# Kernel tuning notes

Measured on AMD Instinct MI355X. Metric: run time of the kernel, lower is better.

## Reference

```python
import jax, jax.numpy as jnp
import numpy as np
from jax import lax

NPOINT = 1024
NSAMPLE = 64
RADIUS = 0.2
EPS = 1e-5  # BatchNorm eps


def farthest_point_sample(xyz, npoint):
    # xyz: [B, N, 3] -> idx [B, npoint]; deterministic init at point 0
    B, N, _ = xyz.shape

    def step(carry, _):
        dist, farthest = carry
        centroid = jnp.take_along_axis(xyz, farthest[:, None, None], axis=1)  # [B,1,3]
        d = jnp.sum((xyz - centroid) ** 2, axis=-1)  # [B,N]
        dist = jnp.minimum(dist, d)
        new_far = jnp.argmax(dist, axis=-1).astype(jnp.int32)
        return (dist, new_far), farthest

    init = (jnp.full((B, N), 1e10, xyz.dtype), jnp.zeros((B,), jnp.int32))
    _, idxs = lax.scan(step, init, None, length=npoint)
    return jnp.transpose(idxs)  # [B, npoint]


def square_distance(src, dst):
    # src [B,S,3], dst [B,N,3] -> [B,S,N]
    d = -2.0 * jnp.einsum('bsc,bnc->bsn', src, dst)
    d += jnp.sum(src ** 2, -1)[:, :, None]
    d += jnp.sum(dst ** 2, -1)[:, None, :]
    return d


def query_ball_point(radius, nsample, xyz, new_xyz):
    B, N, _ = xyz.shape
    sqr = square_distance(new_xyz, xyz)  # [B,S,N]
    gi = jnp.where(sqr > radius ** 2, N, jnp.arange(N, dtype=jnp.int32))
    gi = jnp.sort(gi, axis=-1)[:, :, :nsample]  # [B,S,K]
    first = gi[:, :, :1]
    gi = jnp.where(gi == N, first, gi)
    return gi


def mlp_bn_relu(x, W, g, b):
    # x [B,S,K,Cin], W [Cin,Cout]; 1x1 conv + training-mode BN + ReLU
    y = jnp.einsum('bskc,co->bsko', x, W)
    m = jnp.mean(y, axis=(0, 1, 2))
    v = jnp.var(y, axis=(0, 1, 2))
    y = (y - m) * lax.rsqrt(v + EPS) * g + b
    return jax.nn.relu(y)


def setup_inputs() -> dict:
    key = jax.random.key(0)
    ks = jax.random.split(key, 8)
    B, N, C = 8, 4096, 128
    xyz = jax.random.uniform(ks[0], (B, N, 3), dtype=jnp.float32)
    features = jax.random.normal(ks[1], (B, C, N), dtype=jnp.float32)
    c_in = C + 3  # use_xyz
    W1 = jax.random.normal(ks[2], (c_in, 128), dtype=jnp.float32) * 0.05
    W2 = jax.random.normal(ks[3], (128, 128), dtype=jnp.float32) * 0.05
    W3 = jax.random.normal(ks[4], (128, 256), dtype=jnp.float32) * 0.05
    return {
        'xyz': xyz, 'features': features,
        'W1': W1, 'g1': jnp.ones((128,)), 'b1': jnp.zeros((128,)),
        'W2': W2, 'g2': jnp.ones((128,)), 'b2': jnp.zeros((128,)),
        'W3': W3, 'g3': jnp.ones((256,)), 'b3': jnp.zeros((256,)),
    }


def reference(xyz, features, W1, g1, b1, W2, g2, b2, W3, g3, b3):
    fps_idx = farthest_point_sample(xyz, NPOINT)              # [B,S]
    new_xyz = jnp.take_along_axis(xyz, fps_idx[:, :, None], axis=1)  # [B,S,3]
    gi = query_ball_point(RADIUS, NSAMPLE, xyz, new_xyz)      # [B,S,K]
    gather = jax.vmap(lambda p, i: p[i])                      # per-batch gather
    grouped_xyz = gather(xyz, gi) - new_xyz[:, :, None, :]    # [B,S,K,3]
    grouped_feat = gather(jnp.transpose(features, (0, 2, 1)), gi)  # [B,S,K,C]
    x = jnp.concatenate([grouped_xyz, grouped_feat], axis=-1)  # [B,S,K,3+C]
    x = mlp_bn_relu(x, W1, g1, b1)
    x = mlp_bn_relu(x, W2, g2, b2)
    x = mlp_bn_relu(x, W3, g3, b3)
    new_features = jnp.transpose(jnp.max(x, axis=2), (0, 2, 1))  # [B,256,S]
    return new_xyz, new_features
```

## Files before the change

### kernel.cpp

```cpp
#include <hip/hip_runtime.h>

#define B_  8
#define N_  4096
#define S_  1024
#define K_  64
#define CF_ 128
#define M_  (B_*S_*K_)

typedef __attribute__((ext_vector_type(8))) short bshort8;
typedef __attribute__((ext_vector_type(4))) float f32x4;
typedef __attribute__((ext_vector_type(4))) int   i32x4;
typedef __attribute__((ext_vector_type(2))) float f32x2;
typedef __attribute__((ext_vector_type(4))) unsigned short us4;

__device__ __forceinline__ unsigned short f2bf(float f){
  unsigned int u = __float_as_uint(f);
  u = u + 0x7FFFu + ((u >> 16) & 1u);
  return (unsigned short)(u >> 16);
}
__device__ __forceinline__ float bf2f(unsigned short h){
  return __uint_as_float(((unsigned int)h) << 16);
}

__global__ __launch_bounds__(256) void prep_kernel(const float* __restrict__ f,
                                                   const float* __restrict__ W1,
                                                   const float* __restrict__ W2,
                                                   const float* __restrict__ W3,
                                                   unsigned short* __restrict__ ft,
                                                   unsigned short* __restrict__ Wt1,
                                                   unsigned short* __restrict__ Wt2,
                                                   unsigned short* __restrict__ Wt3){
  __shared__ float tile[32][33];
  const int blk = blockIdx.x;
  if (blk < 4096){
    int nt = blk & 127, ct = (blk>>7)&3, b = blk>>9;
    int tx = threadIdx.x & 31, ty = threadIdx.x >> 5;
#pragma unroll
    for (int r=0; r<32; r+=8)
      tile[ty+r][tx] = f[((size_t)(b*128 + ct*32 + ty + r))*4096 + nt*32 + tx];
    __syncthreads();
#pragma unroll
    for (int r=0; r<32; r+=8){
      int n = nt*32 + ty + r, cc = ct*32 + tx;
      ft[((size_t)b*4096 + n)*128 + cc] = f2bf(tile[tx][ty+r]);
    }
  } else {
    int t = (blk-4096)*256 + threadIdx.x;
    int stride = 64*256;
    for (int idx=t; idx<128*160; idx+=stride){
      int n = idx/160, k = idx-(idx/160)*160;
      float v = 0.f;
      if (k < 128) v = W1[(k+3)*128 + n];
      else if (k < 131) v = W1[(k-128)*128 + n];
      Wt1[idx] = f2bf(v);
    }
    for (int idx=t; idx<128*128; idx+=stride){
      int n = idx>>7, k = idx&127;
      Wt2[idx] = f2bf(W2[k*128+n]);
    }
    for (int idx=t; idx<256*128; idx+=stride){
      int n = idx>>7, k = idx&127;
      Wt3[idx] = f2bf(W3[k*256+n]);
    }
  }
}

__global__ __launch_bounds__(256,2) void pgemm_kernel(const unsigned short* __restrict__ featT,
                                                      const unsigned short* __restrict__ Wt1,
                                                      float* __restrict__ P){
  __shared__ alignas(16) unsigned short At[128*40];
  __shared__ alignas(16) unsigned short Bt[128*40];
  const int t = threadIdx.x, blk = blockIdx.x;
  const size_t rowBase = (size_t)blk*128;
  const int lane = t&63, wave = t>>6;
  const int wm = wave>>1, wn = wave&1;
  const int lrow = lane&15, quad = lane>>4;
  f32x4 acc[4][4];
  const f32x4 z4 = {0.f,0.f,0.f,0.f};
#pragma unroll
  for (int i=0;i<4;++i)
#pragma unroll
    for (int j=0;j<4;++j) acc[i][j]=z4;
  for (int ch=0; ch<4; ++ch){
    __syncthreads();
#pragma unroll
    for (int half=0; half<2; ++half){
      int sl = t + half*256; int r = sl>>2, p = sl&3;
      *(bshort8*)&At[r*40+p*8] = *(const bshort8*)(featT + (rowBase + r)*CF_ + ch*32 + p*8);
      *(bshort8*)&Bt[r*40+p*8] = *(const bshort8*)(Wt1 + r*160 + ch*32 + p*8);
    }
    __syncthreads();
    bshort8 af[4], bfr[4];
#pragma unroll
    for (int mt=0; mt<4; ++mt) af[mt]  = *(const bshort8*)&At[(wm*64+mt*16+lrow)*40 + quad*8];
#pragma unroll
    for (int nt=0; nt<4; ++nt) bfr[nt] = *(const bshort8*)&Bt[(wn*64+nt*16+lrow)*40 + quad*8];
#pragma unroll
    for (int mt=0; mt<4; ++mt)
#pragma unroll
      for (int nt=0; nt<4; ++nt)
        acc[mt][nt] = __builtin_amdgcn_mfma_f32_16x16x32_bf16(af[mt], bfr[nt], acc[mt][nt], 0,0,0);
  }
#pragma unroll
  for (int mt=0; mt<4; ++mt)
#pragma unroll
    for (int nt=0; nt<4; ++nt)
#pragma unroll
      for (int r=0; r<4; ++r){
        int row = wm*64 + mt*16 + quad*4 + r;
        int col = wn*64 + nt*16 + lrow;
        P[(rowBase + row)*128 + col] = acc[mt][nt][r];
      }
}

#define DPP_PAIR_STEP(CTRL)                                                     \
  {                                                                             \
    int _vi = __builtin_amdgcn_update_dpp(__float_as_int(best), __float_as_int(best), (CTRL), 0xF, 0xF, false); \
    int _ii = __builtin_amdgcn_update_dpp(bidx, bidx, (CTRL), 0xF, 0xF, false); \
    float _ov = __int_as_float(_vi);                                            \
    bool _tk = (_ov > best) || (_ov == best && _ii < bidx);                     \
    best = _tk ? _ov : best;                                                    \
    bidx = _tk ? _ii : bidx;                                                    \
  }

__global__ __launch_bounds__(256) void fps_kernel(const float* __restrict__ xyz,
                                                  float* __restrict__ nx_out,
                                                  float* __restrict__ nx_ws){
#pragma clang fp contract(off)
  __shared__ float sx[N_], sy[N_], sz[N_];
  __shared__ int   sidx[S_];
  __shared__ alignas(16) float redv[2][4];
  __shared__ alignas(16) int   redi[2][4];
  const int b = blockIdx.x, t = threadIdx.x;
  const int lane = t & 63, w = t >> 6;
  const float* xb = xyz + (size_t)b*N_*3;
  f32x2 px[8], py[8], pz[8], dist[8];
#pragma unroll
  for (int j=0;j<8;++j){
    int i0 = (2*j)*256 + t, i1 = (2*j+1)*256 + t;
    float x0=xb[i0*3+0], y0=xb[i0*3+1], z0=xb[i0*3+2];
    float x1=xb[i1*3+0], y1=xb[i1*3+1], z1=xb[i1*3+2];
    px[j] = (f32x2){x0,x1}; py[j] = (f32x2){y0,y1}; pz[j] = (f32x2){z0,z1};
    dist[j] = (f32x2){1e10f,1e10f};
    sx[i0]=x0; sy[i0]=y0; sz[i0]=z0;
    sx[i1]=x1; sy[i1]=y1; sz[i1]=z1;
  }
  __syncthreads();
  int farthest = 0;
  float cx = xb[0], cy = xb[1], cz = xb[2];
  for (int it=0; it<S_; ++it){
    if (t==0) sidx[it] = farthest;
    f32x2 cx2 = (f32x2){cx,cx}, cy2 = (f32x2){cy,cy}, cz2 = (f32x2){cz,cz};
    float best = -1.0f; int bidx = 0;
#pragma unroll
    for (int j=0;j<8;++j){
      f32x2 dx = px[j] - cx2;
      f32x2 dy = py[j] - cy2;
      f32x2 dz = pz[j] - cz2;
      f32x2 d  = (dx*dx + dy*dy) + dz*dz;
      f32x2 nd;
      nd.x = fminf(dist[j].x, d.x);
      nd.y = fminf(dist[j].y, d.y);
      dist[j] = nd;
      bool tk0 = nd.x > best;
      best = tk0 ? nd.x : best;
      bidx = tk0 ? ((2*j)*256 + t) : bidx;
      bool tk1 = nd.y > best;
      best = tk1 ? nd.y : best;
      bidx = tk1 ? ((2*j+1)*256 + t) : bidx;
    }
    DPP_PAIR_STEP(0xB1);
    DPP_PAIR_STEP(0x4E);
    DPP_PAIR_STEP(0x124);
    DPP_PAIR_STEP(0x128);
    DPP_PAIR_STEP(0x142);
    DPP_PAIR_STEP(0x143);
    const int buf = it & 1;
    if (lane == 63){ redv[buf][w] = best; redi[buf][w] = bidx; }
    __syncthreads();
    f32x4 vv = *(const f32x4*)&redv[buf][0];
    i32x4 iv = *(const i32x4*)&redi[buf][0];
    float x0=sx[iv[0]], y0=sy[iv[0]], z0=sz[iv[0]];
    float x1=sx[iv[1]], y1=sy[iv[1]], z1=sz[iv[1]];
    float x2=sx[iv[2]], y2=sy[iv[2]], z2=sz[iv[2]];
    float x3=sx[iv[3]], y3=sy[iv[3]], z3=sz[iv[3]];
    float v01 = vv[0]; int i01 = iv[0];
    float cx01 = x0, cy01 = y0, cz01 = z0;
    { bool tk = (vv[1] > v01) || (vv[1] == v01 && iv[1] < i01);
      v01 = tk?vv[1]:v01; i01 = tk?iv[1]:i01;
      cx01 = tk?x1:cx01; cy01 = tk?y1:cy01; cz01 = tk?z1:cz01; }
    float v23 = vv[2]; int i23 = iv[2];
    float cx23 = x2, cy23 = y2, cz23 = z2;
    { bool tk = (vv[3] > v23) || (vv[3] == v23 && iv[3] < i23);
      v23 = tk?vv[3]:v23; i23 = tk?iv[3]:i23;
      cx23 = tk?x3:cx23; cy23 = tk?y3:cy23; cz23 = tk?z3:cz23; }
    { bool tk = (v23 > v01) || (v23 == v01 && i23 < i01);
      v01 = tk?v23:v01; i01 = tk?i23:i01;
      cx01 = tk?cx23:cx01; cy01 = tk?cy23:cy01; cz01 = tk?cz23:cz01; }
    farthest = i01;
    cx = cx01; cy = cy01; cz = cz01;
  }
  __syncthreads();
  for (int i=t; i<S_; i+=256){
    int id = sidx[i];
    size_t base = (size_t)(b*S_+i)*3;
    float vx=sx[id], vy=sy[id], vz=sz[id];
    nx_out[base+0]=vx; nx_out[base+1]=vy; nx_out[base+2]=vz;
    nx_ws[base+0]=vx;  nx_ws[base+1]=vy;  nx_ws[base+2]=vz;
  }
}

__global__ __launch_bounds__(256) void qbp_y1_kernel(const float* __restrict__ xyz,
                                                     const float* __restrict__ nx,
                                                     const float* __restrict__ P,
                                                     const float* __restrict__ W1,
                                                     int* __restrict__ gi,
                                                     float* __restrict__ slots){
  __shared__ int giW[4][64];
  __shared__ alignas(16) float dxL[4][64][4];
  __shared__ float sLDS[128], s2LDS[128];
  const int t = threadIdx.x;
  const int lane = t & 63, w = t >> 6;
  if (t < 128){ sLDS[t]=0.f; s2LDS[t]=0.f; }
  __syncthreads();
  const int wid = blockIdx.x*4 + w;
  const int b = wid >> 10, s = wid & 1023;
  const float* xb = xyz + (size_t)b*N_*3;
  {
    const double R2 = 0.2*0.2;
    const float* c  = nx + (size_t)(b*S_+s)*3;
    double cx=(double)c[0], cy=(double)c[1], cz=(double)c[2];
    double cc = cx*cx + cy*cy + cz*cz;
    int* g = gi + (size_t)(b*S_+s)*K_;
    int count = 0, first = -1;
    for (int ch=0; ch<64 && count<K_; ++ch){
      int i = ch*64 + lane;
      double x = (double)xb[i*3+0], y = (double)xb[i*3+1], z = (double)xb[i*3+2];
      double e  = cx*x + cy*y + cz*z;
      double pp = x*x + y*y + z*z;
      double d  = -2.0*e + cc + pp;
      bool keep = !(d > R2);
      unsigned long long bal = __ballot(keep);
      int pos = count + __builtin_popcountll(bal & ((1ull<<lane)-1ull));
      if (keep && pos < K_){ g[pos] = i; giW[w][pos] = i; }
      if (first < 0 && bal) first = ch*64 + (int)__builtin_ctzll(bal);
      count += __builtin_popcountll(bal);
    }
    if (count < K_){
      int p = count + lane;
      if (p < K_){ g[p] = first; giW[w][p] = first; }
    }
    int i = giW[w][lane];
    const float* pp = xyz + ((size_t)b*N_ + i)*3;
    const float* qq = nx  + (size_t)(b*S_ + s)*3;
    dxL[w][lane][0] = __fsub_rn(pp[0],qq[0]);
    dxL[w][lane][1] = __fsub_rn(pp[1],qq[1]);
    dxL[w][lane][2] = __fsub_rn(pp[2],qq[2]);
  }
  {
    const int cq = lane*2;
    f32x2 w0 = *(const f32x2*)(W1 + cq);
    f32x2 w1v = *(const f32x2*)(W1 + 128 + cq);
    f32x2 w2 = *(const f32x2*)(W1 + 256 + cq);
    f32x2 sA = {0,0}, s2A = {0,0};
#pragma unroll 4
    for (int r=0; r<64; ++r){
      int pi = giW[w][r];
      f32x2 p = *(const f32x2*)(P + ((size_t)b*N_ + pi)*128 + cq);
      float dx = dxL[w][r][0], dy = dxL[w][r][1], dz = dxL[w][r][2];
      f32x2 y;
#pragma unroll
      for (int e=0;e<2;++e)
        y[e] = fmaf(dz, w2[e], fmaf(dy, w1v[e], fmaf(dx, w0[e], p[e])));
      sA.x += y.x; sA.y += y.y;
      s2A.x = fmaf(y.x,y.x,s2A.x); s2A.y = fmaf(y.y,y.y,s2A.y);
    }
    atomicAdd(&sLDS[cq],    sA.x);  atomicAdd(&sLDS[cq+1],  sA.y);
    atomicAdd(&s2LDS[cq],   s2A.x); atomicAdd(&s2LDS[cq+1], s2A.y);
  }
  __syncthreads();
  if (t < 128){
    int slot = blockIdx.x & 63;
    atomicAdd(&slots[(slot*128+t)*2+0], sLDS[t]);
    atomicAdd(&slots[(slot*128+t)*2+1], s2LDS[t]);
  }
}

template<int PHASE, bool STOREY2>
__global__ __launch_bounds__(256,2) void mm_fused(
    const float* __restrict__ P,
    const float* __restrict__ W1,
    const unsigned short* __restrict__ Wt2,
    const unsigned short* __restrict__ Wt3,
    const int* __restrict__ gi,
    const float* __restrict__ xyz,
    const float* __restrict__ nxyz,
    const float* __restrict__ ss1,
    const float* __restrict__ ss2,
    float* __restrict__ slots,
    float* __restrict__ minv,
    float* __restrict__ maxv,
    unsigned short* __restrict__ y2out)
{
  __shared__ alignas(16) unsigned short Bt[2][128*40];
  __shared__ alignas(16) unsigned short Y[128*136];
  __shared__ int giL[128];
  __shared__ alignas(16) float dxL[128][4];
  __shared__ alignas(16) float w0L[128], w1L[128], w2L[128];

  const int t = threadIdx.x;
  const int mblk = blockIdx.x;
  const int b = mblk >> 9;
  const int lane = t&63, wave = t>>6;
  const int wm = wave>>1, wn = wave&1;
  const int lrow = lane&15, quad = lane>>4;
  const int slot = mblk & 63;

  if (t<128){
    int i = gi[(size_t)mblk*128 + t];
    giL[t] = i;
    int s = ((mblk*128 + t) >> 6) & 1023;
    const float* pp = xyz  + ((size_t)b*N_ + i)*3;
    const float* qq = nxyz + (size_t)(b*S_ + s)*3;
    dxL[t][0] = __fsub_rn(pp[0],qq[0]);
    dxL[t][1] = __fsub_rn(pp[1],qq[1]);
    dxL[t][2] = __fsub_rn(pp[2],qq[2]);
    w0L[t] = W1[t]; w1L[t] = W1[128+t]; w2L[t] = W1[256+t];
  }
  __syncthreads();

  {
    const int rgrp = t>>5, cq = (t&31)*4;
    f32x4 w0 = *(const f32x4*)&w0L[cq];
    f32x4 w1 = *(const f32x4*)&w1L[cq];
    f32x4 w2 = *(const f32x4*)&w2L[cq];
    f32x4 a1v = *(const f32x4*)(ss1 + cq);
    f32x4 b1v = *(const f32x4*)(ss1 + 128 + cq);
#pragma unroll
    for (int g=0; g<16; ++g){
      int r = g*8 + rgrp;
      int pi = giL[r];
      f32x4 p = *(const f32x4*)(P + ((size_t)b*N_ + pi)*128 + cq);
      float dx = dxL[r][0], dy = dxL[r][1], dz = dxL[r][2];
      f32x4 y;
#pragma unroll
      for (int e=0;e<4;++e)
        y[e] = fmaf(dz, w2[e], fmaf(dy, w1[e], fmaf(dx, w0[e], p[e])));
      us4 zz;
#pragma unroll
      for (int e=0;e<4;++e)
        zz[e] = f2bf(fmaxf(fmaf(y[e], a1v[e], b1v[e]), 0.f));
      *(us4*)&Y[r*136 + cq] = zz;
    }
  }

  f32x4 acc[4][4];
  const f32x4 z4 = {0.f,0.f,0.f,0.f};
#pragma unroll
  for (int i=0;i<4;++i)
#pragma unroll
    for (int j=0;j<4;++j) acc[i][j]=z4;

  {
    bshort8 bV[2];
#pragma unroll
    for (int half=0; half<2; ++half){
      int sl = t + half*256; int r = sl>>2, p = sl&3;
      bV[half] = *(const bshort8*)(Wt2 + r*128 + p*8);
    }
#pragma unroll
    for (int half=0; half<2; ++half){
      int sl = t + half*256; int r = sl>>2, p = sl&3;
      *(bshort8*)&Bt[1][r*40+p*8] = bV[half];
    }
    for (int ch=0; ch<4; ++ch){
      const int cur = (ch & 1) ^ 1;
      __syncthreads();
      bshort8 af[4], bfr[4];
#pragma unroll
      for (int mt=0; mt<4; ++mt) af[mt]  = *(const bshort8*)&Y[(wm*64+mt*16+lrow)*136 + ch*32 + quad*8];
#pragma unroll
      for (int nt=0; nt<4; ++nt) bfr[nt] = *(const bshort8*)&Bt[cur][(wn*64+nt*16+lrow)*40 + quad*8];
      if (ch < 3){
#pragma unroll
        for (int half=0; half<2; ++half){
          int sl = t + half*256; int r = sl>>2, p = sl&3;
          bV[half] = *(const bshort8*)(Wt2 + r*128 + (ch+1)*32 + p*8);
        }
      }
#pragma unroll
      for (int mt=0; mt<4; ++mt)
#pragma unroll
        for (int nt=0; nt<4; ++nt)
          acc[mt][nt] = __builtin_amdgcn_mfma_f32_16x16x32_bf16(af[mt], bfr[nt], acc[mt][nt], 0,0,0);
      if (ch < 3){
        const int nxt = cur ^ 1;
#pragma unroll
        for (int half=0; half<2; ++half){
          int sl = t + half*256; int r = sl>>2, p = sl&3;
          *(bshort8*)&Bt[nxt][r*40+p*8] = bV[half];
        }
      }
    }
  }

  if constexpr (PHASE==2){
#pragma unroll
    for (int nt=0; nt<4; ++nt){
      float s=0.f, s2=0.f;
#pragma unroll
      for (int mt=0; mt<4; ++mt)
#pragma unroll
        for (int r=0; r<4; ++r){ float v=acc[mt][nt][r]; s+=v; s2=fmaf(v,v,s2); }
      s  += __shfl_xor(s,16,64);  s  += __shfl_xor(s,32,64);
      s2 += __shfl_xor(s2,16,64); s2 += __shfl_xor(s2,32,64);
      if (lane<16){
        int c = wn*64+nt*16+lane;
        atomicAdd(&slots[(slot*128+c)*2+0], s);
        atomicAdd(&slots[(slot*128+c)*2+1], s2);
      }
    }
    if constexpr (STOREY2){
      __syncthreads();
#pragma unroll
      for (int nt=0; nt<4; ++nt){
        int c = wn*64+nt*16+lrow;
#pragma unroll
        for (int mt=0; mt<4; ++mt)
#pragma unroll
          for (int r=0; r<4; ++r){
            int row = wm*64+mt*16+quad*4+r;
            Y[row*136 + c] = f2bf(acc[mt][nt][r]);
          }
      }
      __syncthreads();
      for (int idx=t; idx<128*16; idx+=256){
        int r = idx>>4, p = idx&15;
        bshort8 v = *(const bshort8*)&Y[r*136 + p*8];
        *(bshort8*)(y2out + ((size_t)mblk*128 + r)*128 + p*8) = v;
      }
    }
    return;
  }

  if constexpr (PHASE==3){
    __syncthreads();
#pragma unroll
    for (int nt=0; nt<4; ++nt){
      int c = wn*64+nt*16+lrow;
      float sc = ss2[c], sh = ss2[128+c];
#pragma unroll
      for (int mt=0; mt<4; ++mt)
#pragma unroll
        for (int r=0; r<4; ++r){
          int row = wm*64+mt*16+quad*4+r;
          Y[row*136 + c] = f2bf(fmaxf(fmaf(acc[mt][nt][r], sc, sh), 0.f));
        }
    }

    for (int h=0; h<2; ++h){
#pragma unroll
      for (int i=0;i<4;++i)
#pragma unroll
        for (int j=0;j<4;++j) acc[i][j]=z4;
      bshort8 bV[2];
#pragma unroll
      for (int half=0; half<2; ++half){
        int sl = t + half*256; int r = sl>>2, p = sl&3;
        bV[half] = *(const bshort8*)(Wt3 + ((size_t)(h*128+r))*128 + p*8);
      }
#pragma unroll
      for (int half=0; half<2; ++half){
        int sl = t + half*256; int r = sl>>2, p = sl&3;
        *(bshort8*)&Bt[1][r*40+p*8] = bV[half];
      }
      for (int ch=0; ch<4; ++ch){
        const int cur = (ch & 1) ^ 1;
        __syncthreads();
        bshort8 af[4], bfr[4];
#pragma unroll
        for (int mt=0; mt<4; ++mt) af[mt]  = *(const bshort8*)&Y[(wm*64+mt*16+lrow)*136 + ch*32 + quad*8];
#pragma unroll
        for (int nt=0; nt<4; ++nt) bfr[nt] = *(const bshort8*)&Bt[cur][(wn*64+nt*16+lrow)*40 + quad*8];
        if (ch < 3){
#pragma unroll
          for (int half=0; half<2; ++half){
            int sl = t + half*256; int r = sl>>2, p = sl&3;
            bV[half] = *(const bshort8*)(Wt3 + ((size_t)(h*128+r))*128 + (ch+1)*32 + p*8);
          }
        }
#pragma unroll
        for (int mt=0; mt<4; ++mt)
#pragma unroll
          for (int nt=0; nt<4; ++nt)
            acc[mt][nt] = __builtin_amdgcn_mfma_f32_16x16x32_bf16(af[mt], bfr[nt], acc[mt][nt], 0,0,0);
        if (ch < 3){
          const int nxt = cur ^ 1;
#pragma unroll
          for (int half=0; half<2; ++half){
            int sl = t + half*256; int r = sl>>2, p = sl&3;
            *(bshort8*)&Bt[nxt][r*40+p*8] = bV[half];
          }
        }
      }
#pragma unroll
      for (int nt=0; nt<4; ++nt){
        float s=0.f, s2=0.f, mx=-3.0e38f, mn=3.0e38f;
#pragma unroll
        for (int mt=0; mt<4; ++mt)
#pragma unroll
          for (int r=0; r<4; ++r){
            float v=acc[mt][nt][r];
            s+=v; s2=fmaf(v,v,s2);
            mx=fmaxf(mx,v); mn=fminf(mn,v);
          }
        s  += __shfl_xor(s,16,64);  s  += __shfl_xor(s,32,64);
        s2 += __shfl_xor(s2,16,64); s2 += __shfl_xor(s2,32,64);
        mx = fmaxf(mx, __shfl_xor(mx,16,64)); mx = fmaxf(mx, __shfl_xor(mx,32,64));
        mn = fminf(mn, __shfl_xor(mn,16,64)); mn = fminf(mn, __shfl_xor(mn,32,64));
        if (lane<16){
          int c = h*128 + wn*64+nt*16+lane;
          atomicAdd(&slots[(slot*256+c)*2+0], s);
          atomicAdd(&slots[(slot*256+c)*2+1], s2);
          size_t sidx = (size_t)mblk*2 + wm;
          maxv[sidx*256 + c] = mx;
          minv[sidx*256 + c] = mn;
        }
      }
    }
  }
}

__global__ __launch_bounds__(256,2) void mm3_kernel(
    const unsigned short* __restrict__ y2,
    const unsigned short* __restrict__ Wt3,
    const float* __restrict__ ss2,
    float* __restrict__ slots,
    float* __restrict__ minv,
    float* __restrict__ maxv)
{
  __shared__ alignas(16) unsigned short Bt[2][128*40];
  __shared__ alignas(16) unsigned short Y[128*136];
  const int t = threadIdx.x;
  const int mblk = blockIdx.x;
  const int lane = t&63, wave = t>>6;
  const int wm = wave>>1, wn = wave&1;
  const int lrow = lane&15, quad = lane>>4;
  const int slot = mblk & 63;

  {
    const int rgrp = t>>5, cq = (t&31)*4;
    f32x4 a2 = *(const f32x4*)(ss2 + cq);
    f32x4 b2 = *(const f32x4*)(ss2 + 128 + cq);
#pragma unroll
    for (int g=0; g<16; ++g){
      int r = g*8 + rgrp;
      us4 yv = *(const us4*)(y2 + ((size_t)mblk*128 + r)*128 + cq);
      us4 zz;
#pragma unroll
      for (int e=0;e<4;++e)
        zz[e] = f2bf(fmaxf(fmaf(bf2f(yv[e]), a2[e], b2[e]), 0.f));
      *(us4*)&Y[r*136 + cq] = zz;
    }
  }

  f32x4 acc[4][4];
  const f32x4 z4 = {0.f,0.f,0.f,0.f};
  for (int h=0; h<2; ++h){
#pragma unroll
    for (int i=0;i<4;++i)
#pragma unroll
      for (int j=0;j<4;++j) acc[i][j]=z4;
    bshort8 bV[2];
#pragma unroll
    for (int half=0; half<2; ++half){
      int sl = t + half*256; int r = sl>>2, p = sl&3;
      bV[half] = *(const bshort8*)(Wt3 + ((size_t)(h*128+r))*128 + p*8);
    }
#pragma unroll
    for (int half=0; half<2; ++half){
      int sl = t + half*256; int r = sl>>2, p = sl&3;
      *(bshort8*)&Bt[1][r*40+p*8] = bV[half];
    }
    for (int ch=0; ch<4; ++ch){
      const int cur = (ch & 1) ^ 1;
      __syncthreads();
      bshort8 af[4], bfr[4];
#pragma unroll
      for (int mt=0; mt<4; ++mt) af[mt]  = *(const bshort8*)&Y[(wm*64+mt*16+lrow)*136 + ch*32 + quad*8];
#pragma unroll
      for (int nt=0; nt<4; ++nt) bfr[nt] = *(const bshort8*)&Bt[cur][(wn*64+nt*16+lrow)*40 + quad*8];
      if (ch < 3){
#pragma unroll
        for (int half=0; half<2; ++half){
          int sl = t + half*256; int r = sl>>2, p = sl&3;
          bV[half] = *(const bshort8*)(Wt3 + ((size_t)(h*128+r))*128 + (ch+1)*32 + p*8);
        }
      }
#pragma unroll
      for (int mt=0; mt<4; ++mt)
#pragma unroll
        for (int nt=0; nt<4; ++nt)
          acc[mt][nt] = __builtin_amdgcn_mfma_f32_16x16x32_bf16(af[mt], bfr[nt], acc[mt][nt], 0,0,0);
      if (ch < 3){
        const int nxt = cur ^ 1;
#pragma unroll
        for (int half=0; half<2; ++half){
          int sl = t + half*256; int r = sl>>2, p = sl&3;
          *(bshort8*)&Bt[nxt][r*40+p*8] = bV[half];
        }
      }
    }
#pragma unroll
    for (int nt=0; nt<4; ++nt){
      float s=0.f, s2=0.f, mx=-3.0e38f, mn=3.0e38f;
#pragma unroll
      for (int mt=0; mt<4; ++mt)
#pragma unroll
        for (int r=0; r<4; ++r){
          float v=acc[mt][nt][r];
          s+=v; s2=fmaf(v,v,s2);
          mx=fmaxf(mx,v); mn=fminf(mn,v);
        }
      s  += __shfl_xor(s,16,64);  s  += __shfl_xor(s,32,64);
      s2 += __shfl_xor(s2,16,64); s2 += __shfl_xor(s2,32,64);
      mx = fmaxf(mx, __shfl_xor(mx,16,64)); mx = fmaxf(mx, __shfl_xor(mx,32,64));
      mn = fminf(mn, __shfl_xor(mn,16,64)); mn = fminf(mn, __shfl_xor(mn,32,64));
      if (lane<16){
        int c = h*128 + wn*64+nt*16+lane;
        atomicAdd(&slots[(slot*256+c)*2+0], s);
        atomicAdd(&slots[(slot*256+c)*2+1], s2);
        size_t sidx = (size_t)mblk*2 + wm;
        maxv[sidx*256 + c] = mx;
        minv[sidx*256 + c] = mn;
      }
    }
    if (h==0) __syncthreads();
  }
}

__global__ void stats_kernel(const float* __restrict__ slots, const float* __restrict__ g,
                             const float* __restrict__ beta, float* __restrict__ ssOut,
                             int C, float inv_cnt){
  int c = threadIdx.x;
  if (c >= C) return;
  float s=0.f, s2=0.f;
  for (int k=0;k<64;++k){
    s  += slots[(k*C + c)*2 + 0];
    s2 += slots[(k*C + c)*2 + 1];
  }
  float m = s * inv_cnt;
  float v = fmaxf(s2 * inv_cnt - m*m, 0.f);
  float sc = rsqrtf(v + 1e-5f) * g[c];
  ssOut[c] = sc;
  ssOut[C + c] = beta[c] - m*sc;
}

__global__ __launch_bounds__(256) void final_kernel(const float* __restrict__ minv,
                                                    const float* __restrict__ maxv,
                                                    const float* __restrict__ ss3,
                                                    float* __restrict__ out){
  __shared__ float tile[64][65];
  const int t = threadIdx.x;
  const int cb = blockIdx.x;
  const int sb = blockIdx.y;
  const int b  = blockIdx.z;
  const int w = t>>6, l = t&63;
  {
    int c = cb*64 + l;
    float sc = ss3[c], sh = ss3[256+c];
#pragma unroll
    for (int k=0;k<16;++k){
      int sl = k*4 + w;
      size_t mi = ((size_t)(b*1024 + sb*64 + sl))*256 + c;
      float v = (sc >= 0.f) ? maxv[mi] : minv[mi];
      tile[sl][l] = fmaxf(fmaf(v, sc, sh), 0.f);
    }
  }
  __syncthreads();
#pragma unroll
  for (int k=0;k<16;++k){
    int cl = k*4 + w;
    out[((size_t)(b*256 + cb*64 + cl))*1024 + sb*64 + l] = tile[l][cl];
  }
}

extern "C" void kernel_launch(void* const* d_in, const int* in_sizes, int n_in,
                              void* d_out, int out_size, void* d_ws, size_t ws_size,
                              hipStream_t stream){
  const float* xyz      = (const float*)d_in[0];
  const float* features = (const float*)d_in[1];
  const float* W1 = (const float*)d_in[2];
  const float* g1 = (const float*)d_in[3];
  const float* b1 = (const float*)d_in[4];
  const float* W2 = (const float*)d_in[5];
  const float* g2 = (const float*)d_in[6];
  const float* b2 = (const float*)d_in[7];
  const float* W3 = (const float*)d_in[8];
  const float* g3 = (const float*)d_in[9];
  const float* b3 = (const float*)d_in[10];
  float* out = (float*)d_out;

  char* ws = (char*)d_ws;
  size_t off = 0;
  auto alloc = [&](size_t bytes)->char*{
    char* p = ws + off;
    off = (off + bytes + 255) & ~(size_t)255;
    return p;
  };
  float* slots1 = (float*)alloc((size_t)64*128*2*4);
  float* slots2 = (float*)alloc((size_t)64*128*2*4);
  float* slots3 = (float*)alloc((size_t)64*256*2*4);
  float* ss1    = (float*)alloc(256*4);
  float* ss2    = (float*)alloc(256*4);
  float* ss3    = (float*)alloc(512*4);
  float* nxyz   = (float*)alloc((size_t)24576*4);
  int*   gi     = (int*)  alloc((size_t)M_*4);
  unsigned short* featT = (unsigned short*)alloc((size_t)B_*N_*CF_*2);
  unsigned short* Wt1   = (unsigned short*)alloc((size_t)128*160*2);
  unsigned short* Wt2   = (unsigned short*)alloc((size_t)128*128*2);
  unsigned short* Wt3   = (unsigned short*)alloc((size_t)256*128*2);
  float* minv = (float*)alloc((size_t)B_*S_*256*4);
  float* maxv = (float*)alloc((size_t)B_*S_*256*4);
  float* P    = (float*)alloc((size_t)B_*N_*128*4);
  size_t base_end = off;
  unsigned short* y2 = (unsigned short*)alloc((size_t)M_*128*2);
  const bool bigws = (off <= ws_size);
  (void)base_end;

  hipMemsetAsync(slots1, 0, (size_t)(64*128*2 + 64*128*2 + 64*256*2)*4, stream);

  prep_kernel<<<4160, 256, 0, stream>>>(features, W1, W2, W3, featT, Wt1, Wt2, Wt3);
  pgemm_kernel<<<256, 256, 0, stream>>>(featT, Wt1, P);
  fps_kernel<<<8, 256, 0, stream>>>(xyz, out, nxyz);
  qbp_y1_kernel<<<2048, 256, 0, stream>>>(xyz, nxyz, P, W1, gi, slots1);

  const float inv_cnt = 1.0f / (float)M_;
  stats_kernel<<<1, 128, 0, stream>>>(slots1, g1, b1, ss1, 128, inv_cnt);
  if (bigws){
    mm_fused<2,true><<<4096, 256, 0, stream>>>(P, W1, Wt2, Wt3, gi, xyz, nxyz,
                                               ss1, nullptr, slots2, nullptr, nullptr, y2);
    stats_kernel<<<1, 128, 0, stream>>>(slots2, g2, b2, ss2, 128, inv_cnt);
    mm3_kernel<<<4096, 256, 0, stream>>>(y2, Wt3, ss2, slots3, minv, maxv);
  } else {
    mm_fused<2,false><<<4096, 256, 0, stream>>>(P, W1, Wt2, Wt3, gi, xyz, nxyz,
                                                ss1, nullptr, slots2, nullptr, nullptr, nullptr);
    stats_kernel<<<1, 128, 0, stream>>>(slots2, g2, b2, ss2, 128, inv_cnt);
    mm_fused<3,false><<<4096, 256, 0, stream>>>(P, W1, Wt2, Wt3, gi, xyz, nxyz,
                                                ss1, ss2, slots3, minv, maxv, nullptr);
  }
  stats_kernel<<<1, 256, 0, stream>>>(slots3, g3, b3, ss3, 256, inv_cnt);
  final_kernel<<<dim3(4,16,8), 256, 0, stream>>>(minv, maxv, ss3, out + 24576);
}
```

Baseline: 1.158 ms.

## Single-buffer weight tiles to raise occupancy; reload FPS centroid from LDS

The GEMM kernels drop their double-buffered LDS weight tile and use a single buffer with two barriers per chunk. Launch bounds are raised from 2 to 3 blocks per SM to gain occupancy in exchange for losing the load/compute overlap. In the FPS loop, the winner's coordinates are no longer selected alongside the reduction. Instead they are read from LDS by index at the start of the next iteration, which cuts the per-iteration gathers from twelve to three.

```diff
diff --git a/kernel.cpp b/kernel.cpp
--- a/kernel.cpp
+++ b/kernel.cpp
@@ -147,9 +147,9 @@
   }
   __syncthreads();
   int farthest = 0;
-  float cx = xb[0], cy = xb[1], cz = xb[2];
   for (int it=0; it<S_; ++it){
     if (t==0) sidx[it] = farthest;
+    float cx = sx[farthest], cy = sy[farthest], cz = sz[farthest];
     f32x2 cx2 = (f32x2){cx,cx}, cy2 = (f32x2){cy,cy}, cz2 = (f32x2){cz,cz};
     float best = -1.0f; int bidx = 0;
 #pragma unroll
@@ -180,25 +180,12 @@
     __syncthreads();
     f32x4 vv = *(const f32x4*)&redv[buf][0];
     i32x4 iv = *(const i32x4*)&redi[buf][0];
-    float x0=sx[iv[0]], y0=sy[iv[0]], z0=sz[iv[0]];
-    float x1=sx[iv[1]], y1=sy[iv[1]], z1=sz[iv[1]];
-    float x2=sx[iv[2]], y2=sy[iv[2]], z2=sz[iv[2]];
-    float x3=sx[iv[3]], y3=sy[iv[3]], z3=sz[iv[3]];
     float v01 = vv[0]; int i01 = iv[0];
-    float cx01 = x0, cy01 = y0, cz01 = z0;
-    { bool tk = (vv[1] > v01) || (vv[1] == v01 && iv[1] < i01);
-      v01 = tk?vv[1]:v01; i01 = tk?iv[1]:i01;
-      cx01 = tk?x1:cx01; cy01 = tk?y1:cy01; cz01 = tk?z1:cz01; }
+    { bool tk = (vv[1] > v01) || (vv[1] == v01 && iv[1] < i01); v01 = tk?vv[1]:v01; i01 = tk?iv[1]:i01; }
     float v23 = vv[2]; int i23 = iv[2];
-    float cx23 = x2, cy23 = y2, cz23 = z2;
-    { bool tk = (vv[3] > v23) || (vv[3] == v23 && iv[3] < i23);
-      v23 = tk?vv[3]:v23; i23 = tk?iv[3]:i23;
-      cx23 = tk?x3:cx23; cy23 = tk?y3:cy23; cz23 = tk?z3:cz23; }
-    { bool tk = (v23 > v01) || (v23 == v01 && i23 < i01);
-      v01 = tk?v23:v01; i01 = tk?i23:i01;
-      cx01 = tk?cx23:cx01; cy01 = tk?cy23:cy01; cz01 = tk?cz23:cz01; }
+    { bool tk = (vv[3] > v23) || (vv[3] == v23 && iv[3] < i23); v23 = tk?vv[3]:v23; i23 = tk?iv[3]:i23; }
+    { bool tk = (v23 > v01) || (v23 == v01 && i23 < i01); v01 = tk?v23:v01; i01 = tk?i23:i01; }
     farthest = i01;
-    cx = cx01; cy = cy01; cz = cz01;
   }
   __syncthreads();
   for (int i=t; i<S_; i+=256){
@@ -287,7 +274,7 @@
 }
 
 template<int PHASE, bool STOREY2>
-__global__ __launch_bounds__(256,2) void mm_fused(
+__global__ __launch_bounds__(256,3) void mm_fused(
     const float* __restrict__ P,
     const float* __restrict__ W1,
     const unsigned short* __restrict__ Wt2,
@@ -302,7 +289,7 @@
     float* __restrict__ maxv,
     unsigned short* __restrict__ y2out)
 {
-  __shared__ alignas(16) unsigned short Bt[2][128*40];
+  __shared__ alignas(16) unsigned short Bt[128*40];
   __shared__ alignas(16) unsigned short Y[128*136];
   __shared__ int giL[128];
   __shared__ alignas(16) float dxL[128][4];
@@ -361,47 +348,30 @@
 #pragma unroll
     for (int j=0;j<4;++j) acc[i][j]=z4;
 
-  {
+  for (int ch=0; ch<4; ++ch){
     bshort8 bV[2];
 #pragma unroll
     for (int half=0; half<2; ++half){
       int sl = t + half*256; int r = sl>>2, p = sl&3;
-      bV[half] = *(const bshort8*)(Wt2 + r*128 + p*8);
-    }
+      bV[half] = *(const bshort8*)(Wt2 + r*128 + ch*32 + p*8);
+    }
+    __syncthreads();
 #pragma unroll
     for (int half=0; half<2; ++half){
       int sl = t + half*256; int r = sl>>2, p = sl&3;
-      *(bshort8*)&Bt[1][r*40+p*8] = bV[half];
-    }
-    for (int ch=0; ch<4; ++ch){
-      const int cur = (ch & 1) ^ 1;
-      __syncthreads();
-      bshort8 af[4], bfr[4];
-#pragma unroll
-      for (int mt=0; mt<4; ++mt) af[mt]  = *(const bshort8*)&Y[(wm*64+mt*16+lrow)*136 + ch*32 + quad*8];
-#pragma unroll
-      for (int nt=0; nt<4; ++nt) bfr[nt] = *(const bshort8*)&Bt[cur][(wn*64+nt*16+lrow)*40 + quad*8];
-      if (ch < 3){
-#pragma unroll
-        for (int half=0; half<2; ++half){
-          int sl = t + half*256; int r = sl>>2, p = sl&3;
-          bV[half] = *(const bshort8*)(Wt2 + r*128 + (ch+1)*32 + p*8);
-        }
-      }
-#pragma unroll
-      for (int mt=0; mt<4; ++mt)
-#pragma unroll
-        for (int nt=0; nt<4; ++nt)
-          acc[mt][nt] = __builtin_amdgcn_mfma_f32_16x16x32_bf16(af[mt], bfr[nt], acc[mt][nt], 0,0,0);
-      if (ch < 3){
-        const int nxt = cur ^ 1;
-#pragma unroll
-        for (int half=0; half<2; ++half){
-          int sl = t + half*256; int r = sl>>2, p = sl&3;
-          *(bshort8*)&Bt[nxt][r*40+p*8] = bV[half];
-        }
-      }
-    }
+      *(bshort8*)&Bt[r*40+p*8] = bV[half];
+    }
+    __syncthreads();
+    bshort8 af[4], bfr[4];
+#pragma unroll
+    for (int mt=0; mt<4; ++mt) af[mt]  = *(const bshort8*)&Y[(wm*64+mt*16+lrow)*136 + ch*32 + quad*8];
+#pragma unroll
+    for (int nt=0; nt<4; ++nt) bfr[nt] = *(const bshort8*)&Bt[(wn*64+nt*16+lrow)*40 + quad*8];
+#pragma unroll
+    for (int mt=0; mt<4; ++mt)
+#pragma unroll
+      for (int nt=0; nt<4; ++nt)
+        acc[mt][nt] = __builtin_amdgcn_mfma_f32_16x16x32_bf16(af[mt], bfr[nt], acc[mt][nt], 0,0,0);
   }
 
   if constexpr (PHASE==2){
@@ -463,45 +433,30 @@
       for (int i=0;i<4;++i)
 #pragma unroll
         for (int j=0;j<4;++j) acc[i][j]=z4;
-      bshort8 bV[2];
-#pragma unroll
-      for (int half=0; half<2; ++half){
-        int sl = t + half*256; int r = sl>>2, p = sl&3;
-        bV[half] = *(const bshort8*)(Wt3 + ((size_t)(h*128+r))*128 + p*8);
-      }
-#pragma unroll
-      for (int half=0; half<2; ++half){
-        int sl = t + half*256; int r = sl>>2, p = sl&3;
-        *(bshort8*)&Bt[1][r*40+p*8] = bV[half];
-      }
       for (int ch=0; ch<4; ++ch){
-        const int cur = (ch & 1) ^ 1;
+        bshort8 bV[2];
+#pragma unroll
+        for (int half=0; half<2; ++half){
+          int sl = t + half*256; int r = sl>>2, p = sl&3;
+          bV[half] = *(const bshort8*)(Wt3 + ((size_t)(h*128+r))*128 + ch*32 + p*8);
+        }
+        __syncthreads();
+#pragma unroll
+        for (int half=0; half<2; ++half){
+          int sl = t + half*256; int r = sl>>2, p = sl&3;
+          *(bshort8*)&Bt[r*40+p*8] = bV[half];
+        }
         __syncthreads();
         bshort8 af[4], bfr[4];
 #pragma unroll
         for (int mt=0; mt<4; ++mt) af[mt]  = *(const bshort8*)&Y[(wm*64+mt*16+lrow)*136 + ch*32 + quad*8];
 #pragma unroll
-        for (int nt=0; nt<4; ++nt) bfr[nt] = *(const bshort8*)&Bt[cur][(wn*64+nt*16+lrow)*40 + quad*8];
-        if (ch < 3){
-#pragma unroll
-          for (int half=0; half<2; ++half){
-            int sl = t + half*256; int r = sl>>2, p = sl&3;
-            bV[half] = *(const bshort8*)(Wt3 + ((size_t)(h*128+r))*128 + (ch+1)*32 + p*8);
-          }
-        }
+        for (int nt=0; nt<4; ++nt) bfr[nt] = *(const bshort8*)&Bt[(wn*64+nt*16+lrow)*40 + quad*8];
 #pragma unroll
         for (int mt=0; mt<4; ++mt)
 #pragma unroll
           for (int nt=0; nt<4; ++nt)
             acc[mt][nt] = __builtin_amdgcn_mfma_f32_16x16x32_bf16(af[mt], bfr[nt], acc[mt][nt], 0,0,0);
-        if (ch < 3){
-          const int nxt = cur ^ 1;
-#pragma unroll
-          for (int half=0; half<2; ++half){
-            int sl = t + half*256; int r = sl>>2, p = sl&3;
-            *(bshort8*)&Bt[nxt][r*40+p*8] = bV[half];
-          }
-        }
       }
 #pragma unroll
       for (int nt=0; nt<4; ++nt){
@@ -531,7 +486,7 @@
   }
 }
 
-__global__ __launch_bounds__(256,2) void mm3_kernel(
+__global__ __launch_bounds__(256,3) void mm3_kernel(
     const unsigned short* __restrict__ y2,
     const unsigned short* __restrict__ Wt3,
     const float* __restrict__ ss2,
@@ -539,7 +494,7 @@
     float* __restrict__ minv,
     float* __restrict__ maxv)
 {
-  __shared__ alignas(16) unsigned short Bt[2][128*40];
+  __shared__ alignas(16) unsigned short Bt[128*40];
   __shared__ alignas(16) unsigned short Y[128*136];
   const int t = threadIdx.x;
   const int mblk = blockIdx.x;
@@ -571,45 +526,30 @@
     for (int i=0;i<4;++i)
 #pragma unroll
       for (int j=0;j<4;++j) acc[i][j]=z4;
-    bshort8 bV[2];
-#pragma unroll
-    for (int half=0; half<2; ++half){
-      int sl = t + half*256; int r = sl>>2, p = sl&3;
-      bV[half] = *(const bshort8*)(Wt3 + ((size_t)(h*128+r))*128 + p*8);
-    }
-#pragma unroll
-    for (int half=0; half<2; ++half){
-      int sl = t + half*256; int r = sl>>2, p = sl&3;
-      *(bshort8*)&Bt[1][r*40+p*8] = bV[half];
-    }
     for (int ch=0; ch<4; ++ch){
-      const int cur = (ch & 1) ^ 1;
+      bshort8 bV[2];
+#pragma unroll
+      for (int half=0; half<2; ++half){
+        int sl = t + half*256; int r = sl>>2, p = sl&3;
+        bV[half] = *(const bshort8*)(Wt3 + ((size_t)(h*128+r))*128 + ch*32 + p*8);
+      }
+      __syncthreads();
+#pragma unroll
+      for (int half=0; half<2; ++half){
+        int sl = t + half*256; int r = sl>>2, p = sl&3;
+        *(bshort8*)&Bt[r*40+p*8] = bV[half];
+      }
       __syncthreads();
       bshort8 af[4], bfr[4];
 #pragma unroll
       for (int mt=0; mt<4; ++mt) af[mt]  = *(const bshort8*)&Y[(wm*64+mt*16+lrow)*136 + ch*32 + quad*8];
 #pragma unroll
-      for (int nt=0; nt<4; ++nt) bfr[nt] = *(const bshort8*)&Bt[cur][(wn*64+nt*16+lrow)*40 + quad*8];
-      if (ch < 3){
-#pragma unroll
-        for (int half=0; half<2; ++half){
-          int sl = t + half*256; int r = sl>>2, p = sl&3;
-          bV[half] = *(const bshort8*)(Wt3 + ((size_t)(h*128+r))*128 + (ch+1)*32 + p*8);
-        }
-      }
+      for (int nt=0; nt<4; ++nt) bfr[nt] = *(const bshort8*)&Bt[(wn*64+nt*16+lrow)*40 + quad*8];
 #pragma unroll
       for (int mt=0; mt<4; ++mt)
 #pragma unroll
         for (int nt=0; nt<4; ++nt)
           acc[mt][nt] = __builtin_amdgcn_mfma_f32_16x16x32_bf16(af[mt], bfr[nt], acc[mt][nt], 0,0,0);
-      if (ch < 3){
-        const int nxt = cur ^ 1;
-#pragma unroll
-        for (int half=0; half<2; ++half){
-          int sl = t + half*256; int r = sl>>2, p = sl&3;
-          *(bshort8*)&Bt[nxt][r*40+p*8] = bV[half];
-        }
-      }
     }
 #pragma unroll
     for (int nt=0; nt<4; ++nt){
@@ -635,7 +575,6 @@
         minv[sidx*256 + c] = mn;
       }
     }
-    if (h==0) __syncthreads();
   }
 }
 
```

After: 1.085 ms. 6.3% less time.
